# Kernel tuning notes

Measured on AMD Instinct MI355X. Metric: run time of the kernel, lower is better.

The kernel has to match this reference:

```python
import jax, jax.numpy as jnp
import numpy as np

B, N, C = 4, 2048, 768
H = 12
DH = C // H
HID = 4 * C
EPS = 1e-5


def layer_norm(x, g, b):
    mu = jnp.mean(x, axis=-1, keepdims=True)
    var = jnp.mean(jnp.square(x - mu), axis=-1, keepdims=True)
    return (x - mu) * jax.lax.rsqrt(var + EPS) * g + b


def setup_inputs() -> dict:
    key = jax.random.key(0)
    ks = jax.random.split(key, 8)
    s = 0.02
    return {
        "x": jax.random.normal(ks[0], (B, N, C), dtype=jnp.float32),
        "ln1_g": jnp.ones((C,), jnp.float32),
        "ln1_b": jnp.zeros((C,), jnp.float32),
        # weights stored [in, out] (transpose of torch Linear.weight)
        "w_qkv": jax.random.normal(ks[1], (C, 3 * C), jnp.float32) * s,
        "w_proj": jax.random.normal(ks[2], (C, C), jnp.float32) * s,
        "b_proj": jnp.zeros((C,), jnp.float32),
        "ln2_g": jnp.ones((C,), jnp.float32),
        "ln2_b": jnp.zeros((C,), jnp.float32),
        "w1": jax.random.normal(ks[3], (C, HID), jnp.float32) * s,
        "b1": jnp.zeros((HID,), jnp.float32),
        "w2": jax.random.normal(ks[4], (HID, C), jnp.float32) * s,
        "b2": jnp.zeros((C,), jnp.float32),
    }


def reference(x, ln1_g, ln1_b, w_qkv, w_proj, b_proj, ln2_g, ln2_b, w1, b1, w2, b2):
    # --- attention sub-block (qkv_bias=False, eval mode: dropout/droppath = identity) ---
    h = layer_norm(x, ln1_g, ln1_b)
    qkv = (h @ w_qkv).reshape(B, N, 3, H, DH)          # [B,N,3,H,Dh]
    q, k, v = (qkv[:, :, i].transpose(0, 2, 1, 3) for i in range(3))  # [B,H,N,Dh]
    scale = DH ** -0.5
    attn = jax.nn.softmax(jnp.einsum("bhnd,bhmd->bhnm", q, k) * scale, axis=-1)
    o = jnp.einsum("bhnm,bhmd->bhnd", attn, v).transpose(0, 2, 1, 3).reshape(B, N, C)
    x = x + (o @ w_proj + b_proj)
    # --- MLP sub-block (exact GELU, matching torch nn.GELU) ---
    h2 = layer_norm(x, ln2_g, ln2_b)
    m = jax.nn.gelu(h2 @ w1 + b1, approximate=False) @ w2 + b2
    return x + m
```

## Files before the change

kernel.cpp:

```cpp
#include <hip/hip_runtime.h>
#include <hip/hip_bf16.h>

#define B_ 4
#define N_ 2048
#define C_ 768
#define H_ 12
#define DH_ 64
#define HID_ 3072
#define ROWS_ (B_*N_)

typedef short short8 __attribute__((ext_vector_type(8)));
typedef short short4v __attribute__((ext_vector_type(4)));
typedef unsigned short ushort4v __attribute__((ext_vector_type(4)));
typedef float f32x4 __attribute__((ext_vector_type(4)));

static __device__ __forceinline__ unsigned short f2bf(float f) {
    __hip_bfloat16 h = __float2bfloat16(f);
    unsigned short u;
    __builtin_memcpy(&u, &h, 2);
    return u;
}

static __device__ __forceinline__ void gload16(const unsigned short* g, unsigned short* l) {
    __builtin_amdgcn_global_load_lds(
        (const __attribute__((address_space(1))) unsigned int*)g,
        (__attribute__((address_space(3))) unsigned int*)l, 16, 0, 0);
}

__global__ __launch_bounds__(256, 4) void ln_kernel(
    const float* __restrict__ x, const float* __restrict__ g,
    const float* __restrict__ bta, unsigned short* __restrict__ out) {
    int row = blockIdx.x;
    const float* xr = x + (size_t)row * C_;
    int t = threadIdx.x;
    float v0 = xr[t], v1 = xr[t + 256], v2 = xr[t + 512];
    float s = v0 + v1 + v2, ss = v0*v0 + v1*v1 + v2*v2;
    #pragma unroll
    for (int o = 32; o > 0; o >>= 1) { s += __shfl_down(s, o); ss += __shfl_down(ss, o); }
    __shared__ float red[10];
    int wid = t >> 6;
    if ((t & 63) == 0) { red[wid] = s; red[4 + wid] = ss; }
    __syncthreads();
    if (t == 0) {
        float S = red[0] + red[1] + red[2] + red[3];
        float SS = red[4] + red[5] + red[6] + red[7];
        float mu = S * (1.0f / C_);
        float var = SS * (1.0f / C_) - mu * mu;
        red[8] = mu; red[9] = rsqrtf(var + 1e-5f);
    }
    __syncthreads();
    float mu = red[8], rs = red[9];
    unsigned short* orow = out + (size_t)row * C_;
    orow[t]       = f2bf((v0 - mu) * rs * g[t]       + bta[t]);
    orow[t + 256] = f2bf((v1 - mu) * rs * g[t + 256] + bta[t + 256]);
    orow[t + 512] = f2bf((v2 - mu) * rs * g[t + 512] + bta[t + 512]);
}

__global__ __launch_bounds__(256, 4) void convT_kernel(
    const float* __restrict__ in, unsigned short* __restrict__ out, int K, int NN) {
    __shared__ float tile[32][33];
    int n0 = blockIdx.x * 32, k0 = blockIdx.y * 32;
    int tx = threadIdx.x & 31, ty = threadIdx.x >> 5;
    #pragma unroll
    for (int j = 0; j < 4; j++)
        tile[ty + j*8][tx] = in[(size_t)(k0 + ty + j*8) * NN + n0 + tx];
    __syncthreads();
    #pragma unroll
    for (int j = 0; j < 4; j++)
        out[(size_t)(n0 + ty + j*8) * K + k0 + tx] = f2bf(tile[tx][ty + j*8]);
}

template<int EPI>
__global__ __launch_bounds__(256, 3) void gemm_kernel(
    const unsigned short* __restrict__ A, const unsigned short* __restrict__ Bt,
    int K, int NN,
    const float* __restrict__ bias, const float* __restrict__ res,
    void* __restrict__ outp,
    unsigned short* __restrict__ qo, unsigned short* __restrict__ ko) {
    __shared__ unsigned short Al[128 * 64];
    __shared__ unsigned short Bl[128 * 64];
    const int t = threadIdx.x;
    const int rowA0 = blockIdx.y * 128;
    const int colB0 = blockIdx.x * 128;
    const int wave = t >> 6, lane = t & 63;
    const int wm = wave >> 1, wn = wave & 1;
    const int lr = lane & 15, lg = lane >> 4;

    const unsigned short* Btb = (EPI == 3) ? Bt + (size_t)blockIdx.z * N_ * C_ : Bt;

    f32x4 acc[4][4];
    #pragma unroll
    for (int m = 0; m < 4; m++)
        #pragma unroll
        for (int n = 0; n < 4; n++)
            acc[m][n] = (f32x4){0.f, 0.f, 0.f, 0.f};

    const int srow = wave * 32 + (lane >> 3);
    const int scol = (lane & 7) * 8;
    const unsigned short* Ag = A   + (size_t)(rowA0 + srow) * K + scol;
    const unsigned short* Bg = Btb + (size_t)(colB0 + srow) * K + scol;

    for (int kt = 0; kt < K; kt += 64) {
        __syncthreads();
        #pragma unroll
        for (int j = 0; j < 4; j++) {
            gload16(Ag + (size_t)j * 8 * K + kt, Al + (wave * 32 + j * 8) * 64);
            gload16(Bg + (size_t)j * 8 * K + kt, Bl + (wave * 32 + j * 8) * 64);
        }
        __syncthreads();
        #pragma unroll
        for (int kk = 0; kk < 2; kk++) {
            short8 af[4], bf[4];
            #pragma unroll
            for (int m = 0; m < 4; m++)
                af[m] = *(const short8*)(Al + (wm*64 + m*16 + lr) * 64 + kk*32 + lg*8);
            #pragma unroll
            for (int n = 0; n < 4; n++)
                bf[n] = *(const short8*)(Bl + (wn*64 + n*16 + lr) * 64 + kk*32 + lg*8);
            #pragma unroll
            for (int m = 0; m < 4; m++)
                #pragma unroll
                for (int n = 0; n < 4; n++)
                    acc[m][n] = __builtin_amdgcn_mfma_f32_16x16x32_bf16(af[m], bf[n], acc[m][n], 0, 0, 0);
        }
    }
    #pragma unroll
    for (int m = 0; m < 4; m++) {
        #pragma unroll
        for (int n = 0; n < 4; n++) {
            int gc = colB0 + wn*64 + n*16 + lr;
            #pragma unroll
            for (int r2 = 0; r2 < 4; r2++) {
                int gr = rowA0 + wm*64 + m*16 + lg*4 + r2;
                float val = acc[m][n][r2];
                if (EPI == 0) {
                    int cc = gc - ((gc >= C_) ? C_ : 0);
                    int hh = cc >> 6, d = cc & 63;
                    int bb = gr >> 11, nn2 = gr & 2047;
                    size_t bh = (size_t)bb * H_ + hh;
                    if (gc < C_) qo[(bh * N_ + nn2) * DH_ + d] = f2bf(val * 0.1803368801f);
                    else         ko[(bh * N_ + nn2) * DH_ + d] = f2bf(val);
                } else if (EPI == 1) {
                    size_t idx = (size_t)gr * NN + gc;
                    ((float*)outp)[idx] = res[idx] + val + bias[gc];
                } else if (EPI == 2) {
                    float xg = val + bias[gc];
                    float gl = 0.5f * xg * (1.0f + erff(xg * 0.7071067811865476f));
                    ((unsigned short*)outp)[(size_t)gr * NN + gc] = f2bf(gl);
                } else {
                    size_t vrow = ((size_t)blockIdx.z * H_ + (gr >> 6)) * DH_ + (gr & 63);
                    ((unsigned short*)outp)[vrow * N_ + gc] = f2bf(val);
                }
            }
        }
    }
}

__global__ __launch_bounds__(256, 6) void attn_kernel(
    const unsigned short* __restrict__ q, const unsigned short* __restrict__ k,
    const unsigned short* __restrict__ vt, unsigned short* __restrict__ o) {
    __shared__ unsigned short Kl[64 * 64];
    __shared__ unsigned short Vl[64 * 64];
    const int wgid = blockIdx.x;
    const int c = wgid & 7, idx = wgid >> 3;
    const int bh = c * 6 + (idx >> 5);
    const int qt = idx & 31;
    const int b = bh / H_, h = bh - b * H_;
    const size_t base = (size_t)bh * N_ * DH_;
    const int t = threadIdx.x, wave = t >> 6, lane = t & 63;
    const int lr = lane & 15, lg = lane >> 4;

    const int qrow = qt * 64 + wave * 16 + lr;
    short8 qf[2];
    #pragma unroll
    for (int ks = 0; ks < 2; ks++)
        qf[ks] = *(const short8*)(q + base + (size_t)qrow * DH_ + ks * 32 + lg * 8);

    f32x4 oaccT[4];
    #pragma unroll
    for (int d = 0; d < 4; d++) oaccT[d] = (f32x4){0.f, 0.f, 0.f, 0.f};
    float mi = -1e30f, li = 0.f;

    const int sr0 = t >> 3, sr1 = sr0 + 32, scc = t & 7;
    const unsigned short* kg0 = k  + base + (size_t)sr0 * DH_ + scc * 8;
    const unsigned short* kg1 = k  + base + (size_t)sr1 * DH_ + scc * 8;
    const unsigned short* vg0 = vt + base + (size_t)sr0 * N_  + scc * 8;
    const unsigned short* vg1 = vt + base + (size_t)sr1 * N_  + scc * 8;
    const int sw0 = (scc * 16) ^ ((sr0 & 7) << 4);
    const int sw1 = (scc * 16) ^ ((sr1 & 7) << 4);

    short8 kreg0 = *(const short8*)kg0, kreg1 = *(const short8*)kg1;
    short8 vreg0 = *(const short8*)vg0, vreg1 = *(const short8*)vg1;

    const int NT = N_ / 64;
    for (int kt2 = 0; kt2 < NT; kt2++) {
        __syncthreads();
        *(short8*)((char*)Kl + sr0 * 128 + sw0) = kreg0;
        *(short8*)((char*)Kl + sr1 * 128 + sw1) = kreg1;
        *(short8*)((char*)Vl + sr0 * 128 + sw0) = vreg0;
        *(short8*)((char*)Vl + sr1 * 128 + sw1) = vreg1;
        __syncthreads();
        if (kt2 + 1 < NT) {
            kreg0 = *(const short8*)(kg0 + (size_t)(kt2 + 1) * 64 * DH_);
            kreg1 = *(const short8*)(kg1 + (size_t)(kt2 + 1) * 64 * DH_);
            vreg0 = *(const short8*)(vg0 + (size_t)(kt2 + 1) * 64);
            vreg1 = *(const short8*)(vg1 + (size_t)(kt2 + 1) * 64);
        }
        f32x4 s[4];
        #pragma unroll
        for (int cb = 0; cb < 4; cb++) {
            s[cb] = (f32x4){0.f, 0.f, 0.f, 0.f};
            int key = cb * 16 + lr;
            #pragma unroll
            for (int ks = 0; ks < 2; ks++) {
                int bytecol = ks * 64 + lg * 16;
                short8 kf = *(const short8*)((char*)Kl + key * 128 + (bytecol ^ ((key & 7) << 4)));
                s[cb] = __builtin_amdgcn_mfma_f32_16x16x32_bf16(kf, qf[ks], s[cb], 0, 0, 0);
            }
        }
        float mx = fmaxf(fmaxf(fmaxf(s[0][0], s[0][1]), fmaxf(s[0][2], s[0][3])),
                         fmaxf(fmaxf(s[1][0], s[1][1]), fmaxf(s[1][2], s[1][3])));
        mx = fmaxf(mx, fmaxf(fmaxf(fmaxf(s[2][0], s[2][1]), fmaxf(s[2][2], s[2][3])),
                             fmaxf(fmaxf(s[3][0], s[3][1]), fmaxf(s[3][2], s[3][3]))));
        mx = fmaxf(mx, __shfl_xor(mx, 16));
        mx = fmaxf(mx, __shfl_xor(mx, 32));
        if (__any(mx > mi)) {
            float mn = fmaxf(mi, mx);
            float al = exp2f(mi - mn);
            mi = mn;
            li *= al;
            #pragma unroll
            for (int db = 0; db < 4; db++) oaccT[db] *= al;
        }
        float rs = 0.f;
        #pragma unroll
        for (int cb = 0; cb < 4; cb++)
            #pragma unroll
            for (int i = 0; i < 4; i++) {
                float p = exp2f(s[cb][i] - mi);
                s[cb][i] = p;
                rs += p;
            }
        rs += __shfl_xor(rs, 16);
        rs += __shfl_xor(rs, 32);
        li += rs;
        #pragma unroll
        for (int ks = 0; ks < 2; ks++) {
            short8 pb;
            #pragma unroll
            for (int i = 0; i < 4; i++) {
                pb[i]     = (short)f2bf(s[2*ks][i]);
                pb[i + 4] = (short)f2bf(s[2*ks + 1][i]);
            }
            #pragma unroll
            for (int db = 0; db < 4; db++) {
                int dh = db * 16 + lr;
                int swz = (dh & 7) << 4;
                short4v v0 = *(const short4v*)((char*)Vl + dh * 128 + ((ks * 64 + lg * 8) ^ swz));
                short4v v1 = *(const short4v*)((char*)Vl + dh * 128 + ((ks * 64 + 32 + lg * 8) ^ swz));
                short8 vf;
                #pragma unroll
                for (int i = 0; i < 4; i++) { vf[i] = v0[i]; vf[i + 4] = v1[i]; }
                oaccT[db] = __builtin_amdgcn_mfma_f32_16x16x32_bf16(vf, pb, oaccT[db], 0, 0, 0);
            }
        }
    }
    float inv = 1.0f / li;
    unsigned short* orow = o + ((size_t)b * N_ + qrow) * C_ + h * 64;
    #pragma unroll
    for (int db = 0; db < 4; db++) {
        ushort4v pk;
        #pragma unroll
        for (int i = 0; i < 4; i++) pk[i] = f2bf(oaccT[db][i] * inv);
        *(ushort4v*)(orow + db * 16 + lg * 4) = pk;
    }
}

extern "C" void kernel_launch(void* const* d_in, const int* in_sizes, int n_in,
                              void* d_out, int out_size, void* d_ws, size_t ws_size,
                              hipStream_t stream) {
    (void)in_sizes; (void)n_in; (void)out_size; (void)ws_size;
    const float* x      = (const float*)d_in[0];
    const float* ln1_g  = (const float*)d_in[1];
    const float* ln1_b  = (const float*)d_in[2];
    const float* w_qkv  = (const float*)d_in[3];
    const float* w_proj = (const float*)d_in[4];
    const float* b_proj = (const float*)d_in[5];
    const float* ln2_g  = (const float*)d_in[6];
    const float* ln2_b  = (const float*)d_in[7];
    const float* w1     = (const float*)d_in[8];
    const float* b1     = (const float*)d_in[9];
    const float* w2     = (const float*)d_in[10];
    const float* b2     = (const float*)d_in[11];
    float* out = (float*)d_out;

    char* ws = (char*)d_ws;
    size_t off = 0;
    auto alloc = [&](size_t bytes) {
        char* p = ws + off;
        off += (bytes + 255) & ~(size_t)255;
        return p;
    };
    unsigned short* hb     = (unsigned short*)alloc((size_t)ROWS_ * C_ * 2);
    unsigned short* wqkvT  = (unsigned short*)alloc((size_t)C_ * 3 * C_ * 2);
    unsigned short* wprojT = (unsigned short*)alloc((size_t)C_ * C_ * 2);
    unsigned short* w1T    = (unsigned short*)alloc((size_t)C_ * HID_ * 2);
    unsigned short* w2T    = (unsigned short*)alloc((size_t)HID_ * C_ * 2);
    unsigned short* uni    = (unsigned short*)alloc((size_t)ROWS_ * HID_ * 2);
    unsigned short* qb  = uni;
    unsigned short* kb  = qb  + (size_t)B_ * H_ * N_ * DH_;
    unsigned short* vtb = kb  + (size_t)B_ * H_ * N_ * DH_;
    unsigned short* ob  = vtb + (size_t)B_ * H_ * N_ * DH_;
    unsigned short* mid = uni;

    convT_kernel<<<dim3(3 * C_ / 32, C_ / 32), 256, 0, stream>>>(w_qkv, wqkvT, C_, 3 * C_);
    convT_kernel<<<dim3(C_ / 32, C_ / 32), 256, 0, stream>>>(w_proj, wprojT, C_, C_);
    convT_kernel<<<dim3(HID_ / 32, C_ / 32), 256, 0, stream>>>(w1, w1T, C_, HID_);
    convT_kernel<<<dim3(C_ / 32, HID_ / 32), 256, 0, stream>>>(w2, w2T, HID_, C_);

    ln_kernel<<<ROWS_, 256, 0, stream>>>(x, ln1_g, ln1_b, hb);
    gemm_kernel<0><<<dim3(2 * C_ / 128, ROWS_ / 128), 256, 0, stream>>>(
        hb, wqkvT, C_, 2 * C_, nullptr, nullptr, nullptr, qb, kb);
    gemm_kernel<3><<<dim3(N_ / 128, C_ / 128, B_), 256, 0, stream>>>(
        wqkvT + (size_t)2 * C_ * C_, hb, C_, N_, nullptr, nullptr, (void*)vtb, nullptr, nullptr);
    attn_kernel<<<dim3(8 * 6 * (N_ / 64)), 256, 0, stream>>>(qb, kb, vtb, ob);
    gemm_kernel<1><<<dim3(C_ / 128, ROWS_ / 128), 256, 0, stream>>>(
        ob, wprojT, C_, C_, b_proj, x, (void*)out, nullptr, nullptr);
    ln_kernel<<<ROWS_, 256, 0, stream>>>(out, ln2_g, ln2_b, hb);
    gemm_kernel<2><<<dim3(HID_ / 128, ROWS_ / 128), 256, 0, stream>>>(
        hb, w1T, C_, HID_, b1, nullptr, (void*)mid, nullptr, nullptr);
    gemm_kernel<1><<<dim3(C_ / 128, ROWS_ / 128), 256, 0, stream>>>(
        mid, w2T, HID_, C_, b2, out, (void*)out, nullptr, nullptr);
}
```

Baseline: 461.8 us.

## Process two query sub-tiles per wave in attention to reuse K/V tiles

Each attention workgroup now handles 128 query rows instead of 64, with each wave owning two 16-row query fragments that share the same K and V tiles loaded into LDS. This halves the number of workgroups and the total K/V global loads and LDS writes, and reuses each V fragment read for two MFMAs. It costs more registers (occupancy hint lowered from 6 to 3) and fewer workgroups to fill the GPU.

```diff
diff --git a/kernel.cpp b/kernel.cpp
--- a/kernel.cpp
+++ b/kernel.cpp
@@ -156,30 +156,35 @@
     }
 }
 
-__global__ __launch_bounds__(256, 6) void attn_kernel(
+__global__ __launch_bounds__(256, 3) void attn_kernel(
     const unsigned short* __restrict__ q, const unsigned short* __restrict__ k,
     const unsigned short* __restrict__ vt, unsigned short* __restrict__ o) {
     __shared__ unsigned short Kl[64 * 64];
     __shared__ unsigned short Vl[64 * 64];
     const int wgid = blockIdx.x;
     const int c = wgid & 7, idx = wgid >> 3;
-    const int bh = c * 6 + (idx >> 5);
-    const int qt = idx & 31;
+    const int bh = c * 6 + (idx >> 4);
+    const int qt = idx & 15;
     const int b = bh / H_, h = bh - b * H_;
     const size_t base = (size_t)bh * N_ * DH_;
     const int t = threadIdx.x, wave = t >> 6, lane = t & 63;
     const int lr = lane & 15, lg = lane >> 4;
 
-    const int qrow = qt * 64 + wave * 16 + lr;
-    short8 qf[2];
-    #pragma unroll
-    for (int ks = 0; ks < 2; ks++)
-        qf[ks] = *(const short8*)(q + base + (size_t)qrow * DH_ + ks * 32 + lg * 8);
-
-    f32x4 oaccT[4];
-    #pragma unroll
-    for (int d = 0; d < 4; d++) oaccT[d] = (f32x4){0.f, 0.f, 0.f, 0.f};
-    float mi = -1e30f, li = 0.f;
+    short8 qf[2][2];
+    #pragma unroll
+    for (int ro = 0; ro < 2; ro++) {
+        int qrow = qt * 128 + wave * 32 + ro * 16 + lr;
+        #pragma unroll
+        for (int ks = 0; ks < 2; ks++)
+            qf[ro][ks] = *(const short8*)(q + base + (size_t)qrow * DH_ + ks * 32 + lg * 8);
+    }
+
+    f32x4 oaccT[2][4];
+    float mi[2] = {-1e30f, -1e30f}, li[2] = {0.f, 0.f};
+    #pragma unroll
+    for (int ro = 0; ro < 2; ro++)
+        #pragma unroll
+        for (int d = 0; d < 4; d++) oaccT[ro][d] = (f32x4){0.f, 0.f, 0.f, 0.f};
 
     const int sr0 = t >> 3, sr1 = sr0 + 32, scc = t & 7;
     const unsigned short* kg0 = k  + base + (size_t)sr0 * DH_ + scc * 8;
@@ -206,52 +211,57 @@
             vreg0 = *(const short8*)(vg0 + (size_t)(kt2 + 1) * 64);
             vreg1 = *(const short8*)(vg1 + (size_t)(kt2 + 1) * 64);
         }
-        f32x4 s[4];
-        #pragma unroll
-        for (int cb = 0; cb < 4; cb++) {
-            s[cb] = (f32x4){0.f, 0.f, 0.f, 0.f};
-            int key = cb * 16 + lr;
-            #pragma unroll
-            for (int ks = 0; ks < 2; ks++) {
-                int bytecol = ks * 64 + lg * 16;
-                short8 kf = *(const short8*)((char*)Kl + key * 128 + (bytecol ^ ((key & 7) << 4)));
-                s[cb] = __builtin_amdgcn_mfma_f32_16x16x32_bf16(kf, qf[ks], s[cb], 0, 0, 0);
+        short8 pb[2][2];
+        #pragma unroll
+        for (int ro = 0; ro < 2; ro++) {
+            f32x4 s[4];
+            #pragma unroll
+            for (int cb = 0; cb < 4; cb++) {
+                s[cb] = (f32x4){0.f, 0.f, 0.f, 0.f};
+                int key = cb * 16 + lr;
+                #pragma unroll
+                for (int ks = 0; ks < 2; ks++) {
+                    int bytecol = ks * 64 + lg * 16;
+                    short8 kf = *(const short8*)((char*)Kl + key * 128 + (bytecol ^ ((key & 7) << 4)));
+                    s[cb] = __builtin_amdgcn_mfma_f32_16x16x32_bf16(kf, qf[ro][ks], s[cb], 0, 0, 0);
+                }
             }
-        }
-        float mx = fmaxf(fmaxf(fmaxf(s[0][0], s[0][1]), fmaxf(s[0][2], s[0][3])),
-                         fmaxf(fmaxf(s[1][0], s[1][1]), fmaxf(s[1][2], s[1][3])));
-        mx = fmaxf(mx, fmaxf(fmaxf(fmaxf(s[2][0], s[2][1]), fmaxf(s[2][2], s[2][3])),
-                             fmaxf(fmaxf(s[3][0], s[3][1]), fmaxf(s[3][2], s[3][3]))));
-        mx = fmaxf(mx, __shfl_xor(mx, 16));
-        mx = fmaxf(mx, __shfl_xor(mx, 32));
-        if (__any(mx > mi)) {
-            float mn = fmaxf(mi, mx);
-            float al = exp2f(mi - mn);
-            mi = mn;
-            li *= al;
-            #pragma unroll
-            for (int db = 0; db < 4; db++) oaccT[db] *= al;
-        }
-        float rs = 0.f;
-        #pragma unroll
-        for (int cb = 0; cb < 4; cb++)
-            #pragma unroll
-            for (int i = 0; i < 4; i++) {
-                float p = exp2f(s[cb][i] - mi);
-                s[cb][i] = p;
-                rs += p;
+            float mx = fmaxf(fmaxf(fmaxf(s[0][0], s[0][1]), fmaxf(s[0][2], s[0][3])),
+                             fmaxf(fmaxf(s[1][0], s[1][1]), fmaxf(s[1][2], s[1][3])));
+            mx = fmaxf(mx, fmaxf(fmaxf(fmaxf(s[2][0], s[2][1]), fmaxf(s[2][2], s[2][3])),
+                                 fmaxf(fmaxf(s[3][0], s[3][1]), fmaxf(s[3][2], s[3][3]))));
+            mx = fmaxf(mx, __shfl_xor(mx, 16));
+            mx = fmaxf(mx, __shfl_xor(mx, 32));
+            if (__any(mx > mi[ro])) {
+                float mn = fmaxf(mi[ro], mx);
+                float al = exp2f(mi[ro] - mn);
+                mi[ro] = mn;
+                li[ro] *= al;
+                #pragma unroll
+                for (int db = 0; db < 4; db++) oaccT[ro][db] *= al;
             }
-        rs += __shfl_xor(rs, 16);
-        rs += __shfl_xor(rs, 32);
-        li += rs;
+            float rs = 0.f;
+            #pragma unroll
+            for (int cb = 0; cb < 4; cb++)
+                #pragma unroll
+                for (int i = 0; i < 4; i++) {
+                    float p = exp2f(s[cb][i] - mi[ro]);
+                    s[cb][i] = p;
+                    rs += p;
+                }
+            rs += __shfl_xor(rs, 16);
+            rs += __shfl_xor(rs, 32);
+            li[ro] += rs;
+            #pragma unroll
+            for (int ks = 0; ks < 2; ks++)
+                #pragma unroll
+                for (int i = 0; i < 4; i++) {
+                    pb[ro][ks][i]     = (short)f2bf(s[2*ks][i]);
+                    pb[ro][ks][i + 4] = (short)f2bf(s[2*ks + 1][i]);
+                }
+        }
         #pragma unroll
         for (int ks = 0; ks < 2; ks++) {
-            short8 pb;
-            #pragma unroll
-            for (int i = 0; i < 4; i++) {
-                pb[i]     = (short)f2bf(s[2*ks][i]);
-                pb[i + 4] = (short)f2bf(s[2*ks + 1][i]);
-            }
             #pragma unroll
             for (int db = 0; db < 4; db++) {
                 int dh = db * 16 + lr;
@@ -261,18 +271,23 @@
                 short8 vf;
                 #pragma unroll
                 for (int i = 0; i < 4; i++) { vf[i] = v0[i]; vf[i + 4] = v1[i]; }
-                oaccT[db] = __builtin_amdgcn_mfma_f32_16x16x32_bf16(vf, pb, oaccT[db], 0, 0, 0);
+                oaccT[0][db] = __builtin_amdgcn_mfma_f32_16x16x32_bf16(vf, pb[0][ks], oaccT[0][db], 0, 0, 0);
+                oaccT[1][db] = __builtin_amdgcn_mfma_f32_16x16x32_bf16(vf, pb[1][ks], oaccT[1][db], 0, 0, 0);
             }
         }
     }
-    float inv = 1.0f / li;
-    unsigned short* orow = o + ((size_t)b * N_ + qrow) * C_ + h * 64;
-    #pragma unroll
-    for (int db = 0; db < 4; db++) {
-        ushort4v pk;
-        #pragma unroll
-        for (int i = 0; i < 4; i++) pk[i] = f2bf(oaccT[db][i] * inv);
-        *(ushort4v*)(orow + db * 16 + lg * 4) = pk;
+    #pragma unroll
+    for (int ro = 0; ro < 2; ro++) {
+        float inv = 1.0f / li[ro];
+        int qrow = qt * 128 + wave * 32 + ro * 16 + lr;
+        unsigned short* orow = o + ((size_t)b * N_ + qrow) * C_ + h * 64;
+        #pragma unroll
+        for (int db = 0; db < 4; db++) {
+            ushort4v pk;
+            #pragma unroll
+            for (int i = 0; i < 4; i++) pk[i] = f2bf(oaccT[ro][db][i] * inv);
+            *(ushort4v*)(orow + db * 16 + lg * 4) = pk;
+        }
     }
 }
 
@@ -323,7 +338,7 @@
         hb, wqkvT, C_, 2 * C_, nullptr, nullptr, nullptr, qb, kb);
     gemm_kernel<3><<<dim3(N_ / 128, C_ / 128, B_), 256, 0, stream>>>(
         wqkvT + (size_t)2 * C_ * C_, hb, C_, N_, nullptr, nullptr, (void*)vtb, nullptr, nullptr);
-    attn_kernel<<<dim3(8 * 6 * (N_ / 64)), 256, 0, stream>>>(qb, kb, vtb, ob);
+    attn_kernel<<<dim3(8 * 6 * (N_ / 128)), 256, 0, stream>>>(qb, kb, vtb, ob);
     gemm_kernel<1><<<dim3(C_ / 128, ROWS_ / 128), 256, 0, stream>>>(
         ob, wprojT, C_, C_, b_proj, x, (void*)out, nullptr, nullptr);
     ln_kernel<<<ROWS_, 256, 0, stream>>>(out, ln2_g, ln2_b, hb);
```

After: 445.2 us. 3.6% less time.
